# Optimization experiments

Measured on AMD Instinct MI355X. Metric: run time of the kernel, lower is better.

Reference implementation:

```python
import jax, jax.numpy as jnp
import numpy as np

POOL = 14
NUM_ROIS = 512
H, W, C = 200, 200, 1024


def setup_inputs() -> dict:
    key = jax.random.key(0)
    k1, k2, k3, k4, k5 = jax.random.split(key, 5)
    img = jax.random.normal(k1, (1, H, W, C), dtype=jnp.float32)
    # valid boxes: x + w <= W, y + h <= H, w,h >= 8
    x = jax.random.randint(k2, (1, NUM_ROIS), 0, W // 2)
    y = jax.random.randint(k3, (1, NUM_ROIS), 0, H // 2)
    w = jax.random.randint(k4, (1, NUM_ROIS), 8, W // 2)
    h = jax.random.randint(k5, (1, NUM_ROIS), 8, H // 2)
    rois = jnp.stack([x, y, w, h], axis=-1).astype(jnp.int32)  # [1, R, 4]
    return {"img": img, "rois": rois}


def _roi_resize(fm, box):
    # fm: [H, W, C]; box: [4] int32 (x, y, w, h)
    x, y, w, h = box[0], box[1], box[2], box[3]
    # TF1 tf.image.resize_images bilinear, align_corners=False (asymmetric):
    # src = dst * (in_size / out_size), taps floored + clamped to crop extent.
    sy = jnp.arange(POOL, dtype=jnp.float32) * (h.astype(jnp.float32) / POOL)
    sx = jnp.arange(POOL, dtype=jnp.float32) * (w.astype(jnp.float32) / POOL)
    y0 = jnp.floor(sy).astype(jnp.int32)
    x0 = jnp.floor(sx).astype(jnp.int32)
    y0c = jnp.clip(y0, 0, h - 1)
    y1c = jnp.clip(y0 + 1, 0, h - 1)
    x0c = jnp.clip(x0, 0, w - 1)
    x1c = jnp.clip(x0 + 1, 0, w - 1)
    wy = (sy - y0.astype(jnp.float32))[:, None, None]  # [P,1,1]
    wx = (sx - x0.astype(jnp.float32))[None, :, None]  # [1,P,1]
    iy0, iy1 = y + y0c, y + y1c  # absolute row indices
    ix0, ix1 = x + x0c, x + x1c  # absolute col indices
    g00 = fm[iy0[:, None], ix0[None, :]]  # [P,P,C]
    g01 = fm[iy0[:, None], ix1[None, :]]
    g10 = fm[iy1[:, None], ix0[None, :]]
    g11 = fm[iy1[:, None], ix1[None, :]]
    top = g00 + (g01 - g00) * wx
    bot = g10 + (g11 - g10) * wx
    return top + (bot - top) * wy


def reference(img, rois):
    fm = img[0]  # [H, W, C]
    out = jax.vmap(lambda b: _roi_resize(fm, b))(rois[0])  # [R, P, P, C]
    return out[None]  # [1, R, P, P, C]
```

## Files before the change

kernel.cpp:

```cpp
#include <hip/hip_runtime.h>

#define POOL 14
#define NUM_ROIS 512
#define NUM_ITEMS (NUM_ROIS * POOL)
#define IMG_H 200
#define IMG_W 200
#define IMG_C 1024
#define NUM_XCD 8
#define ROIS_PER_XCD (NUM_ROIS / NUM_XCD)
#define ITEMS_PER_XCD (ROIS_PER_XCD * POOL)
#define XBINS 8
#define NBINS (IMG_H * XBINS)
#define BINS_PER_THREAD 7
#define BLOCKS_PER_XCD 256
#define PERSISTENT_BLOCKS (NUM_XCD * BLOCKS_PER_XCD)

typedef float v4f __attribute__((ext_vector_type(4)));

__device__ __forceinline__ int item_key(const int* __restrict__ rois,
                                        int xcd, int i, int* out_code) {
    const int roi_in = i / POOL;
    const int py     = i - roi_in * POOL;
    const int r      = xcd * ROIS_PER_XCD + roi_in;
    const int4 box   = ((const int4*)rois)[r];
    const float stepy = (float)box.w / (float)POOL;
    const float sy    = (float)py * stepy;
    const int y0  = (int)floorf(sy);
    const int y0c = min(max(y0, 0), box.w - 1);
    const int row = box.y + y0c;
    *out_code = (r << 4) | py;
    return row * XBINS + (box.x >> 5);
}

__global__ __launch_bounds__(256) void order_kernel(
    const int* __restrict__ rois, int* __restrict__ perm) {
    const int xcd = blockIdx.x;
    const int tid = threadIdx.x;
    __shared__ int hist[NBINS];
    __shared__ int cnt[NBINS];
    __shared__ int partial[256];

    for (int k = tid; k < NBINS; k += 256) { hist[k] = 0; cnt[k] = 0; }
    __syncthreads();

    for (int i = tid; i < ITEMS_PER_XCD; i += 256) {
        int code;
        atomicAdd(&hist[item_key(rois, xcd, i, &code)], 1);
    }
    __syncthreads();

    const int b0 = tid * BINS_PER_THREAD;
    int lsum[BINS_PER_THREAD];
    int local = 0;
    for (int j = 0; j < BINS_PER_THREAD; ++j) {
        const int k = b0 + j;
        lsum[j] = local;
        if (k < NBINS) local += hist[k];
    }
    partial[tid] = local;
    __syncthreads();
    for (int off = 1; off < 256; off <<= 1) {
        const int add = (tid >= off) ? partial[tid - off] : 0;
        __syncthreads();
        partial[tid] += add;
        __syncthreads();
    }
    const int chunk_excl = partial[tid] - local;
    for (int j = 0; j < BINS_PER_THREAD; ++j) {
        const int k = b0 + j;
        if (k < NBINS) hist[k] = chunk_excl + lsum[j];
    }
    __syncthreads();

    for (int i = tid; i < ITEMS_PER_XCD; i += 256) {
        int code;
        const int key = item_key(rois, xcd, i, &code);
        const int pos = hist[key] + atomicAdd(&cnt[key], 1);
        perm[xcd * ITEMS_PER_XCD + pos] = code;
    }
}

__device__ __forceinline__ void process_item(
    const float* __restrict__ img, const int* __restrict__ rois,
    float* __restrict__ out, int r, int py, int c)
{
    const int4 box = ((const int4*)rois)[r];
    const int bx = box.x, by = box.y, bw = box.z, bh = box.w;

    const float stepy = (float)bh / (float)POOL;
    const float stepx = (float)bw / (float)POOL;

    const float sy = (float)py * stepy;
    const int   y0 = (int)floorf(sy);
    const float wy = sy - (float)y0;
    const int y0c = min(max(y0, 0), bh - 1);
    const int y1c = min(max(y0 + 1, 0), bh - 1);

    const float* __restrict__ r0c = img + (size_t)(by + y0c) * IMG_W * IMG_C + c;
    const float* __restrict__ r1c = img + (size_t)(by + y1c) * IMG_W * IMG_C + c;
    float* __restrict__ orow =
        out + ((size_t)r * (POOL * POOL) + (size_t)py * POOL) * IMG_C + c;

    int ixa[POOL][2];
    float wxa[POOL];
#pragma unroll
    for (int px = 0; px < POOL; ++px) {
        const float sx = (float)px * stepx;
        const int   x0 = (int)floorf(sx);
        wxa[px]    = sx - (float)x0;
        ixa[px][0] = bx + min(max(x0, 0), bw - 1);
        ixa[px][1] = bx + min(max(x0 + 1, 0), bw - 1);
    }

#pragma unroll
    for (int it = 0; it < POOL / 2; ++it) {
        const int pa = 2 * it, pb = 2 * it + 1;

        const v4f a00 = *(const v4f*)(r0c + (size_t)ixa[pa][0] * IMG_C);
        const v4f a01 = *(const v4f*)(r0c + (size_t)ixa[pa][1] * IMG_C);
        const v4f a10 = *(const v4f*)(r1c + (size_t)ixa[pa][0] * IMG_C);
        const v4f a11 = *(const v4f*)(r1c + (size_t)ixa[pa][1] * IMG_C);
        const v4f b00 = *(const v4f*)(r0c + (size_t)ixa[pb][0] * IMG_C);
        const v4f b01 = *(const v4f*)(r0c + (size_t)ixa[pb][1] * IMG_C);
        const v4f b10 = *(const v4f*)(r1c + (size_t)ixa[pb][0] * IMG_C);
        const v4f b11 = *(const v4f*)(r1c + (size_t)ixa[pb][1] * IMG_C);

        const float wxA = wxa[pa];
        const float wxB = wxa[pb];

        const v4f topA = a00 + (a01 - a00) * wxA;
        const v4f botA = a10 + (a11 - a10) * wxA;
        const v4f resA = topA + (botA - topA) * wy;
        const v4f topB = b00 + (b01 - b00) * wxB;
        const v4f botB = b10 + (b11 - b10) * wxB;
        const v4f resB = topB + (botB - topB) * wy;

        __builtin_nontemporal_store(resA, (v4f*)(orow + (size_t)pa * IMG_C));
        __builtin_nontemporal_store(resB, (v4f*)(orow + (size_t)pb * IMG_C));
    }
}

__global__ __launch_bounds__(256) void roi_row_kernel(
    const float* __restrict__ img,
    const int*   __restrict__ rois,
    const int*   __restrict__ perm,
    float*       __restrict__ out)
{
    const int b   = blockIdx.x;
    const int xcd = b & (NUM_XCD - 1);
    const int pb  = b >> 3;
    const int c   = threadIdx.x * 4;

    for (int t = 0;; ++t) {
        const int idx = t * BLOCKS_PER_XCD + pb;
        if (idx >= ITEMS_PER_XCD) break;
        int r, py;
        if (perm) {
            const int code = perm[xcd * ITEMS_PER_XCD + idx];
            r  = code >> 4;
            py = code & 15;
        } else {
            const int roi_in = idx / POOL;
            py = idx - roi_in * POOL;
            r  = xcd * ROIS_PER_XCD + roi_in;
        }
        process_item(img, rois, out, r, py, c);
    }
}

extern "C" void kernel_launch(void* const* d_in, const int* in_sizes, int n_in,
                              void* d_out, int out_size, void* d_ws, size_t ws_size,
                              hipStream_t stream) {
    const float* img  = (const float*)d_in[0];
    const int*   rois = (const int*)d_in[1];
    float*       out  = (float*)d_out;

    int* perm = nullptr;
    if (d_ws && ws_size >= (size_t)NUM_ITEMS * sizeof(int)) {
        perm = (int*)d_ws;
        order_kernel<<<NUM_XCD, 256, 0, stream>>>(rois, perm);
    }
    roi_row_kernel<<<PERSISTENT_BLOCKS, 256, 0, stream>>>(img, rois, perm, out);
}
```

Before: 591.9 us.

## Use per-XCD atomic work queue for dynamic item scheduling in ROI kernel

Replaces the static strided assignment of sorted ROI rows to persistent blocks with a dynamic work counter per XCD, incremented atomically by each block. The counter is reset inside the ordering kernel. Blocks per XCD drop from 256 to 224, so each CU holds fewer blocks. The aim is to even out load imbalance from rows of unequal cost, at the price of an atomic plus two barriers per item and possibly less locality between blocks that now take non-adjacent rows.

```diff
diff --git a/kernel.cpp b/kernel.cpp
--- a/kernel.cpp
+++ b/kernel.cpp
@@ -12,7 +12,7 @@
 #define XBINS 8
 #define NBINS (IMG_H * XBINS)
 #define BINS_PER_THREAD 7
-#define BLOCKS_PER_XCD 256
+#define BLOCKS_PER_XCD 224
 #define PERSISTENT_BLOCKS (NUM_XCD * BLOCKS_PER_XCD)
 
 typedef float v4f __attribute__((ext_vector_type(4)));
@@ -33,12 +33,15 @@
 }
 
 __global__ __launch_bounds__(256) void order_kernel(
-    const int* __restrict__ rois, int* __restrict__ perm) {
+    const int* __restrict__ rois, int* __restrict__ perm,
+    int* __restrict__ ctr) {
     const int xcd = blockIdx.x;
     const int tid = threadIdx.x;
     __shared__ int hist[NBINS];
     __shared__ int cnt[NBINS];
     __shared__ int partial[256];
+
+    if (tid == 0) ctr[xcd * 32] = 0;
 
     for (int k = tid; k < NBINS; k += 256) { hist[k] = 0; cnt[k] = 0; }
     __syncthreads();
@@ -144,27 +147,31 @@
     const float* __restrict__ img,
     const int*   __restrict__ rois,
     const int*   __restrict__ perm,
+    int*         __restrict__ ctr,
     float*       __restrict__ out)
 {
     const int b   = blockIdx.x;
     const int xcd = b & (NUM_XCD - 1);
-    const int pb  = b >> 3;
     const int c   = threadIdx.x * 4;
 
-    for (int t = 0;; ++t) {
-        const int idx = t * BLOCKS_PER_XCD + pb;
-        if (idx >= ITEMS_PER_XCD) break;
-        int r, py;
-        if (perm) {
+    if (perm) {
+        __shared__ int s_idx;
+        for (;;) {
+            if (threadIdx.x == 0)
+                s_idx = atomicAdd(&ctr[xcd * 32], 1);
+            __syncthreads();
+            const int idx = s_idx;
+            __syncthreads();
+            if (idx >= ITEMS_PER_XCD) break;
             const int code = perm[xcd * ITEMS_PER_XCD + idx];
-            r  = code >> 4;
-            py = code & 15;
-        } else {
+            process_item(img, rois, out, code >> 4, code & 15, c);
+        }
+    } else {
+        for (int idx = b >> 3; idx < ITEMS_PER_XCD; idx += BLOCKS_PER_XCD) {
             const int roi_in = idx / POOL;
-            py = idx - roi_in * POOL;
-            r  = xcd * ROIS_PER_XCD + roi_in;
+            const int py = idx - roi_in * POOL;
+            process_item(img, rois, out, xcd * ROIS_PER_XCD + roi_in, py, c);
         }
-        process_item(img, rois, out, r, py, c);
     }
 }
 
@@ -175,10 +182,13 @@
     const int*   rois = (const int*)d_in[1];
     float*       out  = (float*)d_out;
 
+    const size_t need = (size_t)(NUM_ITEMS + NUM_XCD * 32) * sizeof(int);
     int* perm = nullptr;
-    if (d_ws && ws_size >= (size_t)NUM_ITEMS * sizeof(int)) {
+    int* ctr  = nullptr;
+    if (d_ws && ws_size >= need) {
         perm = (int*)d_ws;
-        order_kernel<<<NUM_XCD, 256, 0, stream>>>(rois, perm);
+        ctr  = perm + NUM_ITEMS;
+        order_kernel<<<NUM_XCD, 256, 0, stream>>>(rois, perm, ctr);
     }
-    roi_row_kernel<<<PERSISTENT_BLOCKS, 256, 0, stream>>>(img, rois, perm, out);
+    roi_row_kernel<<<PERSISTENT_BLOCKS, 256, 0, stream>>>(img, rois, perm, ctr, out);
 }
```

Result: faster. 572.7 us, median of 2 (-3.2%).
